# Kernel optimization log

Measured on AMD Instinct MI355X. Metric: run time of the kernel, lower is better.

The kernel has to match this reference:

```python
import jax, jax.numpy as jnp
import numpy as np

H = 2048   # hidden_size
NH = 16    # num_heads
D = 128    # head_dim_qk == head_dim_v
K = 4      # conv_kernel_size


def _causal_depthwise_conv(x, w, b):
    # x: [B,S,C], w: [C,K], b: [C]. Matches torch Conv1d(groups=C, padding=K-1)[..., :S]
    S = x.shape[1]
    xp = jnp.pad(x, ((0, 0), (K - 1, 0), (0, 0)))
    y = b
    for j in range(K):
        y = y + xp[:, j:j + S, :] * w[:, j]
    return y


def setup_inputs() -> dict:
    key = jax.random.key(0)
    ks = jax.random.split(key, 18)
    s = 0.02
    B, S = 2, 2048
    return {
        "x": jax.random.normal(ks[0], (B, S, H), dtype=jnp.float32),
        "Wq": jax.random.normal(ks[1], (H, NH * D), dtype=jnp.float32) * s,
        "Wk": jax.random.normal(ks[2], (H, NH * D), dtype=jnp.float32) * s,
        "Wv": jax.random.normal(ks[3], (H, NH * D), dtype=jnp.float32) * s,
        "Wa": jax.random.normal(ks[4], (H, NH), dtype=jnp.float32) * s,
        "ba": jax.random.normal(ks[5], (NH,), dtype=jnp.float32) * s,
        "Wb": jax.random.normal(ks[6], (H, NH), dtype=jnp.float32) * s,
        "bb": jax.random.normal(ks[7], (NH,), dtype=jnp.float32) * s,
        "Wg": jax.random.normal(ks[8], (H, NH * D), dtype=jnp.float32) * s,
        "Wo": jax.random.normal(ks[9], (NH * D, H), dtype=jnp.float32) * s,
        "qcw": jax.random.normal(ks[10], (NH * D, K), dtype=jnp.float32) * s,
        "qcb": jax.random.normal(ks[11], (NH * D,), dtype=jnp.float32) * s,
        "kcw": jax.random.normal(ks[12], (NH * D, K), dtype=jnp.float32) * s,
        "kcb": jax.random.normal(ks[13], (NH * D,), dtype=jnp.float32) * s,
        "vcw": jax.random.normal(ks[14], (NH * D, K), dtype=jnp.float32) * s,
        "vcb": jax.random.normal(ks[15], (NH * D,), dtype=jnp.float32) * s,
        "ln_w": jnp.ones((D,), dtype=jnp.float32),
        "ln_b": jnp.zeros((D,), dtype=jnp.float32),
    }


def _forward(x, Wq, Wk, Wv, Wa, ba, Wb, bb, Wg, Wo,
             qcw, qcb, kcw, kcb, vcw, vcb, ln_w, ln_b):
    B, S, _ = x.shape
    q = _causal_depthwise_conv(x @ Wq, qcw, qcb)
    k = _causal_depthwise_conv(x @ Wk, kcw, kcb)
    v = _causal_depthwise_conv(x @ Wv, vcw, vcb)
    q = jax.nn.silu(q).reshape(B, S, NH, D)
    k = jax.nn.silu(k).reshape(B, S, NH, D) * (D ** -0.5)
    v = jax.nn.silu(v).reshape(B, S, NH, D)
    alpha = jax.nn.sigmoid(x @ Wa + ba)  # [B,S,NH]
    beta = jax.nn.sigmoid(x @ Wb + bb)   # [B,S,NH]

    # time-major for scan
    qt = jnp.moveaxis(q, 1, 0)       # [S,B,NH,D]
    kt = jnp.moveaxis(k, 1, 0)
    vt = jnp.moveaxis(v, 1, 0)
    at = jnp.moveaxis(alpha, 1, 0)   # [S,B,NH]
    bt = jnp.moveaxis(beta, 1, 0)

    def step(St, inp):
        q_, k_, v_, a_, b_ = inp
        sk = jnp.einsum('bhij,bhj->bhi', St, k_)            # [B,NH,D]
        err = sk - v_
        Sn = (a_[..., None, None] * St
              - b_[..., None, None] * err[..., None] * k_[..., None, :])
        o_ = jnp.einsum('bhij,bhj->bhi', Sn, q_)
        return Sn, o_

    S0 = jnp.zeros((B, NH, D, D), dtype=x.dtype)
    _, o = jax.lax.scan(step, S0, (qt, kt, vt, at, bt))
    o = jnp.moveaxis(o, 0, 1)  # [B,S,NH,D]

    # LayerNorm over head_dim
    mu = jnp.mean(o, axis=-1, keepdims=True)
    var = jnp.mean(jnp.square(o - mu), axis=-1, keepdims=True)
    o = (o - mu) * jax.lax.rsqrt(var + 1e-5) * ln_w + ln_b

    g = jax.nn.sigmoid(x @ Wg).reshape(B, S, NH, D)
    o = (o * g).reshape(B, S, NH * D)
    return o @ Wo


def reference(x, Wq, Wk, Wv, Wa, ba, Wb, bb, Wg, Wo,
              qcw, qcb, kcw, kcb, vcw, vcb, ln_w, ln_b):
    return _forward(x, Wq, Wk, Wv, Wa, ba, Wb, bb, Wg, Wo,
                    qcw, qcb, kcw, kcb, vcw, vcb, ln_w, ln_b)
```

## Files before the change

### kernel.cpp

```cpp
#include <hip/hip_runtime.h>
#include <math.h>
#include <stdint.h>

typedef unsigned short u16;
typedef unsigned int u32;
typedef __attribute__((ext_vector_type(8))) short short8;
typedef __attribute__((ext_vector_type(4))) float f32x4;

#define MFMA16(a, b, c) __builtin_amdgcn_mfma_f32_16x16x32_bf16(a, b, c, 0, 0, 0)

__device__ __forceinline__ u16 f2bf(float f) {
  union { float f; u32 u; } v; v.f = f;
  return (u16)((v.u + 0x7FFFu + ((v.u >> 16) & 1u)) >> 16);
}
__device__ __forceinline__ float bf2f(u16 h) {
  union { u32 u; float f; } v; v.u = ((u32)h) << 16; return v.f;
}
__device__ __forceinline__ float bflo(u32 p) {
  union { u32 u; float f; } v; v.u = p << 16; return v.f;
}
__device__ __forceinline__ float bfhi(u32 p) {
  union { u32 u; float f; } v; v.u = p & 0xffff0000u; return v.f;
}
__device__ __forceinline__ float sigm(float x) { return 1.f / (1.f + expf(-x)); }

__global__ void k_cvt_x(const float* __restrict__ x, u16* __restrict__ xb) {
  int i = (blockIdx.x * 256 + threadIdx.x) * 8;
  float4 a = *(const float4*)(x + i);
  float4 b = *(const float4*)(x + i + 4);
  uint4 p;
  p.x = (u32)f2bf(a.x) | ((u32)f2bf(a.y) << 16);
  p.y = (u32)f2bf(a.z) | ((u32)f2bf(a.w) << 16);
  p.z = (u32)f2bf(b.x) | ((u32)f2bf(b.y) << 16);
  p.w = (u32)f2bf(b.z) | ((u32)f2bf(b.w) << 16);
  *(uint4*)(xb + i) = p;
}

__global__ void k_tconv4(const float* __restrict__ W0, const float* __restrict__ W1,
                         const float* __restrict__ W2, const float* __restrict__ W3,
                         u16* __restrict__ Wt) {
  __shared__ float tile[32][33];
  int z = blockIdx.z;
  const float* W = (z == 0) ? W0 : (z == 1) ? W1 : (z == 2) ? W2 : W3;
  u16* dst = Wt + (size_t)z * 2048 * 2048;
  int n0 = blockIdx.x * 32, k0 = blockIdx.y * 32;
  int tc = threadIdx.x & 31, tr = threadIdx.x >> 5;
  #pragma unroll
  for (int p = 0; p < 4; ++p) {
    int k = k0 + p * 8 + tr;
    tile[p * 8 + tr][tc] = W[(size_t)k * 2048 + n0 + tc];
  }
  __syncthreads();
  #pragma unroll
  for (int p = 0; p < 4; ++p) {
    int n = n0 + p * 8 + tr;
    dst[(size_t)n * 2048 + k0 + tc] = f2bf(tile[tc][p * 8 + tr]);
  }
}

__global__ void k_tconv(const float* __restrict__ W, u16* __restrict__ Wt) {
  __shared__ float tile[32][33];
  int n0 = blockIdx.x * 32, k0 = blockIdx.y * 32;
  int tc = threadIdx.x & 31, tr = threadIdx.x >> 5;
  #pragma unroll
  for (int p = 0; p < 4; ++p) {
    int k = k0 + p * 8 + tr;
    tile[p * 8 + tr][tc] = W[(size_t)k * 2048 + n0 + tc];
  }
  __syncthreads();
  #pragma unroll
  for (int p = 0; p < 4; ++p) {
    int n = n0 + p * 8 + tr;
    Wt[(size_t)n * 2048 + k0 + tc] = f2bf(tile[tc][p * 8 + tr]);
  }
}

__global__ __launch_bounds__(256)
void k_ab(const float* __restrict__ x, const float* __restrict__ Wa,
          const float* __restrict__ ba, const float* __restrict__ Wb,
          const float* __restrict__ bb, float* __restrict__ ab2) {
  __shared__ float Wl[128 * 32];
  __shared__ float xl[8][128];
  const int t = threadIdx.x;
  const int lr = t >> 5, c = t & 31;
  const int r0 = blockIdx.x * 8;
  const int ch = c & 15;
  const float* Wsrc = (c < 16) ? Wa : Wb;
  float acc = 0.f;
  for (int kt = 0; kt < 16; ++kt) {
    #pragma unroll
    for (int i = 0; i < 16; ++i) {
      int idx = i * 256 + t;
      int kk = idx >> 5, cc = idx & 31;
      const float* Ws = (cc < 16) ? Wa : Wb;
      Wl[kk * 32 + cc] = Ws[(kt * 128 + kk) * 16 + (cc & 15)];
    }
    #pragma unroll
    for (int i = 0; i < 4; ++i) {
      int idx = i * 256 + t;
      int rr = idx >> 7, kk = idx & 127;
      xl[rr][kk] = x[(size_t)(r0 + rr) * 2048 + kt * 128 + kk];
    }
    __syncthreads();
    #pragma unroll
    for (int kk = 0; kk < 128; kk += 4) {
      float2 x01 = *(const float2*)&xl[lr][kk];
      float2 x23 = *(const float2*)&xl[lr][kk + 2];
      acc += x01.x * Wl[(kk + 0) * 32 + c] + x01.y * Wl[(kk + 1) * 32 + c]
           + x23.x * Wl[(kk + 2) * 32 + c] + x23.y * Wl[(kk + 3) * 32 + c];
    }
    __syncthreads();
  }
  acc += (c < 16) ? ba[ch] : bb[ch];
  float sg = sigm(acc);
  int rowi = r0 + lr;
  int b = rowi >> 11, s = rowi & 2047;
  size_t base = ((size_t)(b * 16 + ch) * 2048 + s) * 2;
  if (c < 16) ab2[base + 0] = sg;
  else        ab2[base + 1] = sg;
}

__device__ __forceinline__ void gld_lds16(const u16* g, u16* l) {
  __builtin_amdgcn_global_load_lds((const __attribute__((address_space(1))) void*)g,
                                   (__attribute__((address_space(3))) void*)l, 16, 0, 0);
}

template <int MODE>
__global__ void k_gemm(const u16* __restrict__ A, const u16* __restrict__ Bw,
                       void* C0, void* C1, int Kd) {
  __shared__ u16 As[2][128 * 32];
  __shared__ u16 Bs[2][128 * 32];
  const int t = threadIdx.x;
  const int lane = t & 63, wv = t >> 6;
  const int wr = wv >> 1, wc = wv & 1;
  const int m0 = blockIdx.y * 128, n0 = blockIdx.x * 128;
  f32x4 acc[4][4] = {};
  const int NT = Kd / 32;

  auto stage = [&](int buf, int kt) {
    #pragma unroll
    for (int i = 0; i < 2; ++i) {
      int li = i * 256 + t;
      int row = li >> 2, kc = li & 3;
      int kcs = kc ^ ((row >> 1) & 3);
      const u16* ga = A + (size_t)(m0 + row) * Kd + kt * 32 + kcs * 8;
      gld_lds16(ga, &As[buf][(i * 256 + wv * 64) * 8]);
      const u16* gb = Bw + (size_t)(n0 + row) * Kd + kt * 32 + kcs * 8;
      gld_lds16(gb, &Bs[buf][(i * 256 + wv * 64) * 8]);
    }
  };

  stage(0, 0);
  __syncthreads();
  int buf = 0;
  const int l15 = lane & 15, l4 = lane >> 4;
  for (int kt = 0; kt < NT; ++kt) {
    if (kt + 1 < NT) stage(buf ^ 1, kt + 1);
    short8 af[4], bfr[4];
    #pragma unroll
    for (int m = 0; m < 4; ++m) {
      int row = wr * 64 + m * 16 + l15;
      int g = l4 ^ ((row >> 1) & 3);
      af[m] = *(const short8*)&As[buf][row * 32 + g * 8];
    }
    #pragma unroll
    for (int n = 0; n < 4; ++n) {
      int row = wc * 64 + n * 16 + l15;
      int g = l4 ^ ((row >> 1) & 3);
      bfr[n] = *(const short8*)&Bs[buf][row * 32 + g * 8];
    }
    #pragma unroll
    for (int m = 0; m < 4; ++m)
      #pragma unroll
      for (int n = 0; n < 4; ++n)
        acc[m][n] = MFMA16(af[m], bfr[n], acc[m][n]);
    __syncthreads();
    buf ^= 1;
  }
  #pragma unroll
  for (int m = 0; m < 4; ++m)
    #pragma unroll
    for (int n = 0; n < 4; ++n)
      #pragma unroll
      for (int e = 0; e < 4; ++e) {
        int row = m0 + wr * 64 + m * 16 + l4 * 4 + e;
        int col = n0 + wc * 64 + n * 16 + l15;
        if (MODE == 0) {
          ((float*)C0)[(size_t)row * 2048 + col] = acc[m][n][e];
        } else {
          u16 vb = f2bf(acc[m][n][e]);
          if (n0 < 6144) ((u16*)C0)[(size_t)row * 6144 + col] = vb;
          else           ((u16*)C1)[(size_t)row * 2048 + (col - 6144)] = vb;
        }
      }
}

template <int MODE>
__global__ __launch_bounds__(512)
void k_gemm8(const u16* __restrict__ A, const u16* __restrict__ Bw,
             void* C0, void* C1) {
  __shared__ u16 lds[65536];
  const int t = threadIdx.x;
  const int w = t >> 6, lane = t & 63;
  const int l15 = lane & 15, l4 = lane >> 4;
  const int wm = w >> 2, wn = w & 3;
  const int bid = blockIdx.x;
  const int mt = ((bid & 7) << 1) | ((bid >> 3) & 1);
  const int nt = bid >> 4;
  const int m0 = mt * 256, n0 = nt * 256;

  f32x4 acc[8][4] = {};
  short8 a[4][2], b[4][2];

  auto stageHalf = [&](int buf, int kt, int mat, int half) {
    const u16* src = mat ? Bw : A;
    const int row0 = (mat ? n0 : m0) + half * 128;
    u16* dst0 = &lds[mat * 32768 + (buf * 2 + half) * 8192 + w * 1024];
    #pragma unroll
    for (int i = 0; i < 2; ++i) {
      int f = w * 128 + i * 64 + lane;
      int rr = f >> 3, g = f & 7;
      const u16* ga = src + (size_t)(row0 + rr) * 2048 + kt * 64 + ((g ^ (rr & 7)) << 3);
      gld_lds16(ga, dst0 + i * 512);
    }
  };
  auto rdA = [&](int buf, int mq, int ks) {
    int row = wm * 64 + (mq & 3) * 16 + l15;
    int g = (l4 + ks * 4) ^ (row & 7);
    return *(const short8*)&lds[(buf * 2 + (mq >> 2)) * 8192 + row * 64 + g * 8];
  };
  auto rdB = [&](int buf, int n, int ks) {
    int row = wn * 32 + (n & 1) * 16 + l15;
    int g = (l4 + ks * 4) ^ (row & 7);
    return *(const short8*)&lds[32768 + (buf * 2 + (n >> 1)) * 8192 + row * 64 + g * 8];
  };

  stageHalf(0, 0, 0, 0); stageHalf(0, 0, 1, 0);
  stageHalf(0, 0, 1, 1); stageHalf(0, 0, 0, 1);
  asm volatile("s_waitcnt vmcnt(0)" ::: "memory");
  __builtin_amdgcn_s_barrier();
  __builtin_amdgcn_sched_barrier(0);

  for (int kt = 0; kt < 32; ++kt) {
    const int bufc = kt & 1, bufn = bufc ^ 1;
    const int ktn = (kt + 1 < 32) ? kt + 1 : 31;

    #pragma unroll
    for (int mq = 0; mq < 4; ++mq) { a[mq][0] = rdA(bufc, mq, 0); a[mq][1] = rdA(bufc, mq, 1); }
    #pragma unroll
    for (int n = 0; n < 2; ++n) { b[n][0] = rdB(bufc, n, 0); b[n][1] = rdB(bufc, n, 1); }
    stageHalf(bufn, ktn, 0, 0);
    __builtin_amdgcn_s_barrier();
    asm volatile("s_waitcnt lgkmcnt(0)" ::: "memory");
    __builtin_amdgcn_sched_barrier(0);
    __builtin_amdgcn_s_setprio(1);
    #pragma unroll
    for (int mq = 0; mq < 4; ++mq)
      #pragma unroll
      for (int n = 0; n < 2; ++n) {
        acc[mq][n] = MFMA16(a[mq][0], b[n][0], acc[mq][n]);
        acc[mq][n] = MFMA16(a[mq][1], b[n][1], acc[mq][n]);
      }
    __builtin_amdgcn_s_setprio(0);
    asm volatile("s_waitcnt vmcnt(4)" ::: "memory");
    __builtin_amdgcn_s_barrier();
    __builtin_amdgcn_sched_barrier(0);

    #pragma unroll
    for (int n = 2; n < 4; ++n) { b[n][0] = rdB(bufc, n, 0); b[n][1] = rdB(bufc, n, 1); }
    stageHalf(bufn, ktn, 1, 0);
    __builtin_amdgcn_s_barrier();
    asm volatile("s_waitcnt lgkmcnt(0)" ::: "memory");
    __builtin_amdgcn_sched_barrier(0);
    __builtin_amdgcn_s_setprio(1);
    #pragma unroll
    for (int mq = 0; mq < 4; ++mq)
      #pragma unroll
      for (int n = 2; n < 4; ++n) {
        acc[mq][n] = MFMA16(a[mq][0], b[n][0], acc[mq][n]);
        acc[mq][n] = MFMA16(a[mq][1], b[n][1], acc[mq][n]);
      }
    __builtin_amdgcn_s_setprio(0);
    asm volatile("s_waitcnt vmcnt(4)" ::: "memory");
    __builtin_amdgcn_s_barrier();
    __builtin_amdgcn_sched_barrier(0);

    #pragma unroll
    for (int mq = 0; mq < 4; ++mq) { a[mq][0] = rdA(bufc, mq + 4, 0); a[mq][1] = rdA(bufc, mq + 4, 1); }
    stageHalf(bufn, ktn, 1, 1);
    __builtin_amdgcn_s_barrier();
    asm volatile("s_waitcnt lgkmcnt(0)" ::: "memory");
    __builtin_amdgcn_sched_barrier(0);
    __builtin_amdgcn_s_setprio(1);
    #pragma unroll
    for (int mq = 0; mq < 4; ++mq)
      #pragma unroll
      for (int n = 2; n < 4; ++n) {
        acc[mq + 4][n] = MFMA16(a[mq][0], b[n][0], acc[mq + 4][n]);
        acc[mq + 4][n] = MFMA16(a[mq][1], b[n][1], acc[mq + 4][n]);
      }
    __builtin_amdgcn_s_setprio(0);
    __builtin_amdgcn_s_barrier();
    __builtin_amdgcn_sched_barrier(0);

    stageHalf(bufn, ktn, 0, 1);
    __builtin_amdgcn_s_barrier();
    asm volatile("s_waitcnt lgkmcnt(0)" ::: "memory");
    __builtin_amdgcn_sched_barrier(0);
    __builtin_amdgcn_s_setprio(1);
    #pragma unroll
    for (int mq = 0; mq < 4; ++mq)
      #pragma unroll
      for (int n = 0; n < 2; ++n) {
        acc[mq + 4][n] = MFMA16(a[mq][0], b[n][0], acc[mq + 4][n]);
        acc[mq + 4][n] = MFMA16(a[mq][1], b[n][1], acc[mq + 4][n]);
      }
    __builtin_amdgcn_s_setprio(0);
    asm volatile("s_waitcnt vmcnt(4)" ::: "memory");
    __builtin_amdgcn_s_barrier();
    __builtin_amdgcn_sched_barrier(0);
  }

  const bool toG = (MODE == 1) && (n0 >= 6144);
  #pragma unroll
  for (int mq = 0; mq < 8; ++mq) {
    int row = m0 + (mq >> 2) * 128 + wm * 64 + (mq & 3) * 16 + l4 * 4;
    #pragma unroll
    for (int n = 0; n < 4; ++n) {
      int col = n0 + (n >> 1) * 128 + wn * 32 + (n & 1) * 16 + l15;
      #pragma unroll
      for (int e = 0; e < 4; ++e) {
        if (MODE == 0) {
          ((float*)C0)[(size_t)(row + e) * 2048 + col] = acc[mq][n][e];
        } else {
          u16 vb = f2bf(acc[mq][n][e]);
          if (!toG) ((u16*)C0)[(size_t)(row + e) * 6144 + col] = vb;
          else      ((u16*)C1)[(size_t)(row + e) * 2048 + (col - 6144)] = vb;
        }
      }
    }
  }
}

__global__ void k_conv(const u16* __restrict__ projQKV,
                       const float* __restrict__ qcw, const float* __restrict__ qcb,
                       const float* __restrict__ kcw, const float* __restrict__ kcb,
                       const float* __restrict__ vcw, const float* __restrict__ vcb,
                       u16* __restrict__ qkv2) {
  int idx = blockIdx.x * 256 + threadIdx.x;
  int cq = idx % 1536, rrow = idx / 1536;
  int c = cq * 4;
  int s = rrow & 2047, b = rrow >> 11;
  int type = c >> 11;
  int ch = c & 2047;
  int h = ch >> 7, d = ch & 127;
  const float* cw; const float* cb;
  if (type == 0)      { cw = qcw; cb = qcb; }
  else if (type == 1) { cw = kcw; cb = kcb; }
  else                { cw = vcw; cb = vcb; }
  float wch[4][4];
  #pragma unroll
  for (int u = 0; u < 4; ++u) {
    float4 wv = *(const float4*)(cw + (ch + u) * 4);
    wch[u][0] = wv.x; wch[u][1] = wv.y; wch[u][2] = wv.z; wch[u][3] = wv.w;
  }
  float4 bv = *(const float4*)(cb + ch);
  float accv[4] = {bv.x, bv.y, bv.z, bv.w};
  #pragma unroll
  for (int j = 0; j < 4; ++j) {
    int sj = s - 3 + j;
    if (sj < 0) continue;
    const u16* p = projQKV + (size_t)(rrow + j - 3) * 6144 + c;
    u32 pa = *(const u32*)p;
    u32 pb = *(const u32*)(p + 2);
    accv[0] += bflo(pa) * wch[0][j];
    accv[1] += bfhi(pa) * wch[1][j];
    accv[2] += bflo(pb) * wch[2][j];
    accv[3] += bfhi(pb) * wch[3][j];
  }
  u16 o4[4];
  #pragma unroll
  for (int u = 0; u < 4; ++u) {
    float y = accv[u];
    float sv = y * sigm(y);
    if (type == 1) sv *= 0.08838834764831845f;
    o4[u] = f2bf(sv);
  }
  int off = (type == 1 ? 0 : (type == 0 ? 128 : 256)) + d;
  u16* dst = qkv2 + ((size_t)(b * 16 + h) * 2048 + s) * 384 + off;
  *(u32*)dst       = (u32)o4[0] | ((u32)o4[1] << 16);
  *(u32*)(dst + 2) = (u32)o4[2] | ((u32)o4[3] << 16);
}

__global__ __launch_bounds__(256)
void k_chunkA(const u16* __restrict__ qkv2, const float* __restrict__ ab2,
              u16* __restrict__ Tbv, u16* __restrict__ nTbk,
              u16* __restrict__ Aq, float* __restrict__ vecs,
              u16* __restrict__ Kt) {
  __shared__ u16 Kl[64][136], Ql[64][136];
  __shared__ float Gk[4096], Gq[4096];
  __shared__ float clL[64], laL[64], bL[64], gpL[64];
  const int unit = blockIdx.x;
  const int bh = unit >> 5, c = unit & 31;
  const int t = threadIdx.x;
  const int wv = t >> 6, lane = t & 63;
  const int l15 = lane & 15, l4 = lane >> 4;
  const u16* qb = qkv2 + ((size_t)bh * 2048 + c * 64) * 384;

  #pragma unroll
  for (int p = 0; p < 4; ++p) {
    int ld = p * 256 + t;
    int row = ld >> 4, c8 = (ld & 15) * 8;
    *(uint4*)&Kl[row][c8] = *(const uint4*)(qb + (size_t)row * 384 + c8);
    *(uint4*)&Ql[row][c8] = *(const uint4*)(qb + (size_t)row * 384 + 128 + c8);
  }
  if (wv == 0) {
    float2 abv = *(const float2*)(ab2 + ((size_t)bh * 2048 + c * 64 + lane) * 2);
    float la = log2f(abv.x);
    float cl = la;
    #pragma unroll
    for (int o = 1; o < 64; o <<= 1) {
      float nv = __shfl_up(cl, o, 64);
      if (lane >= o) cl += nv;
    }
    clL[lane] = cl; laL[lane] = la; bL[lane] = abv.y;
    gpL[lane] = exp2f(cl - la);
  }
  __syncthreads();

  {
    const int t0 = (wv >> 1) * 32, i0 = (wv & 1) * 32;
    f32x4 ak[2][2] = {}, aq[2][2] = {};
    #pragma unroll
    for (int ks = 0; ks < 4; ++ks) {
      short8 bk[2], Ka[2], Qa[2];
      #pragma unroll
      for (int n = 0; n < 2; ++n)
        bk[n] = *(const short8*)&Kl[i0 + n * 16 + l15][ks * 32 + l4 * 8];
      #pragma unroll
      for (int m = 0; m < 2; ++m) {
        Ka[m] = *(const short8*)&Kl[t0 + m * 16 + l15][ks * 32 + l4 * 8];
        Qa[m] = *(const short8*)&Ql[t0 + m * 16 + l15][ks * 32 + l4 * 8];
      }
      #pragma unroll
      for (int m = 0; m < 2; ++m)
        #pragma unroll
        for (int n = 0; n < 2; ++n) {
          ak[m][n] = MFMA16(Ka[m], bk[n], ak[m][n]);
          aq[m][n] = MFMA16(Qa[m], bk[n], aq[m][n]);
        }
    }
    #pragma unroll
    for (int m = 0; m < 2; ++m)
      #pragma unroll
      for (int n = 0; n < 2; ++n)
        #pragma unroll
        for (int e = 0; e < 4; ++e) {
          int row = t0 + m * 16 + l4 * 4 + e;
          int col = i0 + n * 16 + l15;
          Gk[row * 64 + col] = ak[m][n][e];
          Gq[row * 64 + col] = aq[m][n][e];
        }
  }
  __syncthreads();

  #pragma unroll
  for (int p = 0; p < 16; ++p) {
    int e = p * 256 + t; int tt = e >> 6, ii = e & 63;
    float lv = 0.f;
    if (ii < tt) lv = bL[tt] * Gk[e] * exp2f(clL[tt] - laL[tt] - clL[ii]);
    float av = (ii <= tt) ? Gq[e] * exp2f(clL[tt] - clL[ii]) : 0.f;
    Gk[e] = lv;
    Aq[(size_t)unit * 4096 + e] = f2bf(av);
  }
  __syncthreads();

  float X[64];
  if (t < 128) {
    #pragma unroll
    for (int r = 0; r < 64; ++r)
      X[r] = bL[r] * bf2f(qb[(size_t)r * 384 + 256 + t]);
  } else {
    int ck = t - 128;
    #pragma unroll
    for (int r = 0; r < 64; ++r)
      X[r] = -bL[r] * gpL[r] * bf2f(Kl[r][ck]);
  }
  #pragma unroll
  for (int i = 0; i < 63; ++i) {
    float xi = X[i];
    #pragma unroll
    for (int r = i + 1; r < 64; ++r)
      X[r] = fmaf(-Gk[r * 64 + i], xi, X[r]);
  }
  if (t < 128) {
    #pragma unroll
    for (int r = 0; r < 64; ++r)
      Tbv[(size_t)unit * 8192 + r * 128 + t] = f2bf(X[r]);
  } else {
    #pragma unroll
    for (int r = 0; r < 64; ++r)
      nTbk[(size_t)unit * 8192 + r * 128 + (t - 128)] = f2bf(X[r]);
  }
  if (t < 64) {
    vecs[(size_t)unit * 128 + t] = exp2f(clL[t]);
    vecs[(size_t)unit * 128 + 64 + t] = exp2f(clL[63] - clL[t]);
  }
  {
    int dk = t >> 1, tt0 = (t & 1) * 32;
    uint4 w[4];
    u16* wp = (u16*)w;
    #pragma unroll
    for (int j = 0; j < 32; ++j) wp[j] = Kl[tt0 + j][dk];
    uint4* dst = (uint4*)(Kt + (size_t)unit * 8192 + dk * 64 + tt0);
    dst[0] = w[0]; dst[1] = w[1]; dst[2] = w[2]; dst[3] = w[3];
  }
}

#define OFF_NT  0
#define OFF_AQ  8192
#define OFF_Q   12288
#define OFF_KT  20480
#define OFF_TBV 28672
#define STG_U16 29696

__global__ __launch_bounds__(256)
void k_chunkB(const u16* __restrict__ qkv2, const u16* __restrict__ Tbv,
              const u16* __restrict__ nTbk, const u16* __restrict__ Aq,
              const u16* __restrict__ Kt, const float* __restrict__ vecs,
              float* __restrict__ o) {
  __shared__ u16 stg[2][STG_U16];
  __shared__ float S[16 * 132];
  __shared__ u16 Ut[16 * 72], Utd[16 * 72];
  __shared__ float gdl[2][128];
  const int bid = blockIdx.x;
  const int xcd = bid & 7, within = bid >> 3;
  const int sl = within & 7, hgrp = within >> 3;
  const int bh = hgrp * 8 + xcd;
  const int dv0 = sl * 16;
  const int b = bh >> 4, h = bh & 15;
  const int t = threadIdx.x;
  const int wv = t >> 6, lane = t & 63;
  const int l15 = lane & 15, l4 = lane >> 4;
  const int t0 = wv * 16;
  const int dk0 = wv * 32;
  const u16* qbase = qkv2 + (size_t)bh * 2048 * 384;
  float* obase = o + (size_t)b * 2048 * 2048 + h * 128 + dv0;

  for (int p = t; p < 16 * 132; p += 256) S[p] = 0.f;

  auto stage = [&](int buf, int c) {
    u16* sb = &stg[buf][0];
    const size_t unit = (size_t)bh * 32 + c;
    const u16* tbk = nTbk + unit * 8192;
    const u16* aqp = Aq + unit * 4096;
    const u16* ktp = Kt + unit * 8192;
    const u16* tbv = Tbv + unit * 8192;
    const u16* qp  = qbase + (size_t)c * 64 * 384 + 128;
    #pragma unroll
    for (int r = 0; r < 4; ++r) {
      int f = r * 256 + t; int rr = f >> 4, c16 = f & 15;
      gld_lds16(tbk + rr * 128 + (c16 ^ (rr & 7)) * 8, sb + OFF_NT + (r * 256 + wv * 64) * 8);
    }
    #pragma unroll
    for (int r = 0; r < 2; ++r) {
      int f = r * 256 + t; int rr = f >> 3, c8 = f & 7;
      gld_lds16(aqp + rr * 64 + (c8 ^ (rr & 7)) * 8, sb + OFF_AQ + (r * 256 + wv * 64) * 8);
    }
    #pragma unroll
    for (int r = 0; r < 4; ++r) {
      int f = r * 256 + t; int rr = f >> 4, c16 = f & 15;
      gld_lds16(qp + rr * 384 + (c16 ^ (rr & 7)) * 8, sb + OFF_Q + (r * 256 + wv * 64) * 8);
    }
    #pragma unroll
    for (int r = 0; r < 4; ++r) {
      int f = r * 256 + t; int rr = f >> 3, c8 = f & 7;
      gld_lds16(ktp + rr * 64 + (c8 ^ (rr & 7)) * 8, sb + OFF_KT + (r * 256 + wv * 64) * 8);
    }
    if (t < 128)
      gld_lds16(tbv + (t >> 1) * 128 + dv0 + (t & 1) * 8, sb + OFF_TBV + wv * 64 * 8);
  };

  stage(0, 0);
  if (t < 128) gdl[0][t] = vecs[(size_t)bh * 32 * 128 + t];
  __syncthreads();

  for (int c = 0; c < 32; ++c) {
    const int buf = c & 1;
    const u16* sb = &stg[buf][0];
    float vnext = 0.f;
    if (c + 1 < 32) {
      stage(buf ^ 1, c + 1);
      if (t < 128) vnext = vecs[((size_t)bh * 32 + c + 1) * 128 + t];
    }

    f32x4 acc1 = {}, acc2 = {};
    #pragma unroll
    for (int e = 0; e < 4; ++e)
      acc1[e] = bf2f(sb[OFF_TBV + (t0 + l4 * 4 + e) * 16 + l15]);
    #pragma unroll
    for (int ks = 0; ks < 4; ++ks) {
      short8 bhi, blo;
      {
        const float* srow = &S[l15 * 132 + ks * 32 + l4 * 8];
        float4 s0 = *(const float4*)srow, s1 = *(const float4*)(srow + 4);
        float sv[8] = {s0.x, s0.y, s0.z, s0.w, s1.x, s1.y, s1.z, s1.w};
        #pragma unroll
        for (int j = 0; j < 8; ++j) {
          u16 hv = f2bf(sv[j]);
          bhi[j] = (short)hv;
          blo[j] = (short)f2bf(sv[j] - bf2f(hv));
        }
      }
      const int cx = ((ks * 4 + l4) ^ (l15 & 7)) * 8;
      short8 a1 = *(const short8*)&sb[OFF_NT + (t0 + l15) * 128 + cx];
      short8 a2 = *(const short8*)&sb[OFF_Q + (t0 + l15) * 128 + cx];
      acc1 = MFMA16(a1, bhi, acc1);
      acc1 = MFMA16(a1, blo, acc1);
      acc2 = MFMA16(a2, bhi, acc2);
      acc2 = MFMA16(a2, blo, acc2);
    }
    {
      u16 up[4], ud[4];
      #pragma unroll
      for (int e = 0; e < 4; ++e) {
        float uv = acc1[e];
        up[e] = f2bf(uv);
        ud[e] = f2bf(uv * gdl[buf][64 + t0 + l4 * 4 + e]);
      }
      int ux = l15 * 72 + t0 + l4 * 4;
      *(u32*)&Ut[ux]      = (u32)up[0] | ((u32)up[1] << 16);
      *(u32*)&Ut[ux + 2]  = (u32)up[2] | ((u32)up[3] << 16);
      *(u32*)&Utd[ux]     = (u32)ud[0] | ((u32)ud[1] << 16);
      *(u32*)&Utd[ux + 2] = (u32)ud[2] | ((u32)ud[3] << 16);
    }
    asm volatile("s_waitcnt lgkmcnt(0)" ::: "memory");
    __builtin_amdgcn_s_barrier();
    __builtin_amdgcn_sched_barrier(0);

    #pragma unroll
    for (int e = 0; e < 4; ++e) acc2[e] *= gdl[buf][t0 + l4 * 4 + e];
    #pragma unroll
    for (int ks = 0; ks < 2; ++ks) {
      const int cx = ((ks * 4 + l4) ^ (l15 & 7)) * 8;
      short8 af = *(const short8*)&sb[OFF_AQ + (t0 + l15) * 64 + cx];
      short8 bf_ = *(const short8*)&Ut[l15 * 72 + ks * 32 + l4 * 8];
      acc2 = MFMA16(af, bf_, acc2);
    }
    #pragma unroll
    for (int e = 0; e < 4; ++e)
      obase[(size_t)(c * 64 + t0 + l4 * 4 + e) * 2048 + l15] = acc2[e];

    f32x4 acc3[2] = {};
    #pragma unroll
    for (int ks = 0; ks < 2; ++ks) {
      short8 a3 = *(const short8*)&Utd[l15 * 72 + ks * 32 + l4 * 8];
      #pragma unroll
      for (int n = 0; n < 2; ++n) {
        const int kr = dk0 + n * 16 + l15;
        const int cx = ((ks * 4 + l4) ^ (l15 & 7)) * 8;
        short8 b3 = *(const short8*)&sb[OFF_KT + kr * 64 + cx];
        acc3[n] = MFMA16(a3, b3, acc3[n]);
      }
    }
    float gtot = gdl[buf][63];
    #pragma unroll
    for (int n = 0; n < 2; ++n)
      #pragma unroll
      for (int e = 0; e < 4; ++e) {
        float* sp = &S[(l4 * 4 + e) * 132 + dk0 + n * 16 + l15];
        *sp = gtot * *sp + acc3[n][e];
      }
    if (c + 1 < 32 && t < 128) gdl[buf ^ 1][t] = vnext;
    __syncthreads();
  }
}

__global__ void k_lng(const float* __restrict__ o, const u16* __restrict__ projG,
                      const float* __restrict__ ln_w, const float* __restrict__ ln_b,
                      u16* __restrict__ og) {
  int gidx = blockIdx.x * 4 + (threadIdx.x >> 6);
  int lane = threadIdx.x & 63;
  int rrow = gidx >> 4, h = gidx & 15;
  const float* op = o + (size_t)rrow * 2048 + h * 128;
  float2 x2 = *(const float2*)(op + lane * 2);
  float sum = x2.x + x2.y, sq = x2.x * x2.x + x2.y * x2.y;
  #pragma unroll
  for (int m = 1; m < 64; m <<= 1) {
    sum += __shfl_xor(sum, m, 64);
    sq  += __shfl_xor(sq, m, 64);
  }
  float mu = sum * (1.f / 128.f);
  float var = sq * (1.f / 128.f) - mu * mu;
  float rs = 1.0f / sqrtf(var + 1e-5f);
  u32 gu = *(const u32*)(projG + (size_t)rrow * 2048 + h * 128 + lane * 2);
  float g0 = sigm(bflo(gu)), g1 = sigm(bfhi(gu));
  int d0 = lane * 2;
  float y0 = ((x2.x - mu) * rs * ln_w[d0] + ln_b[d0]) * g0;
  float y1 = ((x2.y - mu) * rs * ln_w[d0 + 1] + ln_b[d0 + 1]) * g1;
  *(u32*)(og + (size_t)rrow * 2048 + h * 128 + d0) = (u32)f2bf(y0) | ((u32)f2bf(y1) << 16);
}

extern "C" void kernel_launch(void* const* d_in, const int* in_sizes, int n_in,
                              void* d_out, int out_size, void* d_ws, size_t ws_size,
                              hipStream_t stream) {
  const float* x   = (const float*)d_in[0];
  const float* Wq  = (const float*)d_in[1];
  const float* Wk  = (const float*)d_in[2];
  const float* Wv  = (const float*)d_in[3];
  const float* Wa  = (const float*)d_in[4];
  const float* ba  = (const float*)d_in[5];
  const float* Wb  = (const float*)d_in[6];
  const float* bb  = (const float*)d_in[7];
  const float* Wg  = (const float*)d_in[8];
  const float* Wo  = (const float*)d_in[9];
  const float* qcw = (const float*)d_in[10];
  const float* qcb = (const float*)d_in[11];
  const float* kcw = (const float*)d_in[12];
  const float* kcb = (const float*)d_in[13];
  const float* vcw = (const float*)d_in[14];
  const float* vcb = (const float*)d_in[15];
  const float* lnw = (const float*)d_in[16];
  const float* lnb = (const float*)d_in[17];
  float* out = (float*)d_out;

  if (ws_size < 168820736ull) return;
  char* ws = (char*)d_ws;
  u16*   xb   = (u16*)(ws);
  u16*   Kt   = (u16*)(ws);
  u16*   og   = (u16*)(ws);
  u16*   Wt   = (u16*)(ws + 16777216);
  u16*   Wot  = (u16*)(ws + 16777216);
  u16*   Tbv  = (u16*)(ws + 25165824);
  u16*   Aq   = (u16*)(ws + 41943040);
  u16*   pQKV = (u16*)(ws + 50331648);
  float* oB   = (float*)(ws + 50331648);
  u16*   nTbk = (u16*)(ws + 83886080);
  u16*   pG   = (u16*)(ws + 100663296);
  u16*   qkv2 = (u16*)(ws + 117440512);
  float* ab2  = (float*)(ws + 167772160);
  float* vecs = (float*)(ws + 168296448);

  k_cvt_x<<<4096, 256, 0, stream>>>(x, xb);
  k_tconv4<<<dim3(64, 64, 4), 256, 0, stream>>>(Wq, Wk, Wv, Wg, Wt);
  k_ab<<<512, 256, 0, stream>>>(x, Wa, ba, Wb, bb, ab2);

  k_gemm8<1><<<512, 512, 0, stream>>>(xb, Wt, pQKV, pG);
  k_tconv<<<dim3(64, 64), 256, 0, stream>>>(Wo, Wot);
  k_conv<<<24576, 256, 0, stream>>>(pQKV, qcw, qcb, kcw, kcb, vcw, vcb, qkv2);
  k_chunkA<<<1024, 256, 0, stream>>>(qkv2, ab2, Tbv, nTbk, Aq, vecs, Kt);
  k_chunkB<<<256, 256, 0, stream>>>(qkv2, Tbv, nTbk, Aq, Kt, vecs, oB);
  k_lng<<<16384, 256, 0, stream>>>(oB, pG, lnw, lnb, og);
  k_gemm<0><<<dim3(16, 32), 256, 0, stream>>>(og, Wot, out, nullptr, 2048);
}
```

Before: 466.9 us.

## Restructure GEMM main loop into two phases with fewer barriers

Restructures the GEMM k-loop from four sub-phases with eight barriers per iteration to two phases. Three of the four next-tile stage loads now issue up front and the last goes out mid-iteration, each followed by a larger MFMA block covering all four B fragments. The aim is to cut barrier and lgkmcnt wait overhead and give the scheduler bigger MFMA runs. In exchange the code holds all B fragments in registers at once and relies on the vmcnt(6)/vmcnt(2) counts being right. Removing the explicit lgkmcnt waits and intermediate barriers risks LDS read/write ordering hazards between buffers. It also drops an unused variable in k_ab.

```diff
diff --git a/kernel.cpp b/kernel.cpp
--- a/kernel.cpp
+++ b/kernel.cpp
@@ -85,7 +85,6 @@
   const int lr = t >> 5, c = t & 31;
   const int r0 = blockIdx.x * 8;
   const int ch = c & 15;
-  const float* Wsrc = (c < 16) ? Wa : Wb;
   float acc = 0.f;
   for (int kt = 0; kt < 16; ++kt) {
     #pragma unroll
@@ -245,78 +244,39 @@
     const int bufc = kt & 1, bufn = bufc ^ 1;
     const int ktn = (kt + 1 < 32) ? kt + 1 : 31;
 
+    stageHalf(bufn, ktn, 0, 0);
+    stageHalf(bufn, ktn, 1, 0);
+    stageHalf(bufn, ktn, 1, 1);
     #pragma unroll
     for (int mq = 0; mq < 4; ++mq) { a[mq][0] = rdA(bufc, mq, 0); a[mq][1] = rdA(bufc, mq, 1); }
     #pragma unroll
-    for (int n = 0; n < 2; ++n) { b[n][0] = rdB(bufc, n, 0); b[n][1] = rdB(bufc, n, 1); }
-    stageHalf(bufn, ktn, 0, 0);
-    __builtin_amdgcn_s_barrier();
-    asm volatile("s_waitcnt lgkmcnt(0)" ::: "memory");
-    __builtin_amdgcn_sched_barrier(0);
+    for (int n = 0; n < 4; ++n) { b[n][0] = rdB(bufc, n, 0); b[n][1] = rdB(bufc, n, 1); }
     __builtin_amdgcn_s_setprio(1);
     #pragma unroll
     for (int mq = 0; mq < 4; ++mq)
       #pragma unroll
-      for (int n = 0; n < 2; ++n) {
+      for (int n = 0; n < 4; ++n) {
         acc[mq][n] = MFMA16(a[mq][0], b[n][0], acc[mq][n]);
         acc[mq][n] = MFMA16(a[mq][1], b[n][1], acc[mq][n]);
       }
     __builtin_amdgcn_s_setprio(0);
-    asm volatile("s_waitcnt vmcnt(4)" ::: "memory");
+    asm volatile("s_waitcnt vmcnt(6)" ::: "memory");
     __builtin_amdgcn_s_barrier();
     __builtin_amdgcn_sched_barrier(0);
 
-    #pragma unroll
-    for (int n = 2; n < 4; ++n) { b[n][0] = rdB(bufc, n, 0); b[n][1] = rdB(bufc, n, 1); }
-    stageHalf(bufn, ktn, 1, 0);
-    __builtin_amdgcn_s_barrier();
-    asm volatile("s_waitcnt lgkmcnt(0)" ::: "memory");
-    __builtin_amdgcn_sched_barrier(0);
+    stageHalf(bufn, ktn, 0, 1);
+    #pragma unroll
+    for (int mq = 0; mq < 4; ++mq) { a[mq][0] = rdA(bufc, mq + 4, 0); a[mq][1] = rdA(bufc, mq + 4, 1); }
     __builtin_amdgcn_s_setprio(1);
     #pragma unroll
     for (int mq = 0; mq < 4; ++mq)
       #pragma unroll
-      for (int n = 2; n < 4; ++n) {
-        acc[mq][n] = MFMA16(a[mq][0], b[n][0], acc[mq][n]);
-        acc[mq][n] = MFMA16(a[mq][1], b[n][1], acc[mq][n]);
-      }
-    __builtin_amdgcn_s_setprio(0);
-    asm volatile("s_waitcnt vmcnt(4)" ::: "memory");
-    __builtin_amdgcn_s_barrier();
-    __builtin_amdgcn_sched_barrier(0);
-
-    #pragma unroll
-    for (int mq = 0; mq < 4; ++mq) { a[mq][0] = rdA(bufc, mq + 4, 0); a[mq][1] = rdA(bufc, mq + 4, 1); }
-    stageHalf(bufn, ktn, 1, 1);
-    __builtin_amdgcn_s_barrier();
-    asm volatile("s_waitcnt lgkmcnt(0)" ::: "memory");
-    __builtin_amdgcn_sched_barrier(0);
-    __builtin_amdgcn_s_setprio(1);
-    #pragma unroll
-    for (int mq = 0; mq < 4; ++mq)
-      #pragma unroll
-      for (int n = 2; n < 4; ++n) {
+      for (int n = 0; n < 4; ++n) {
         acc[mq + 4][n] = MFMA16(a[mq][0], b[n][0], acc[mq + 4][n]);
         acc[mq + 4][n] = MFMA16(a[mq][1], b[n][1], acc[mq + 4][n]);
       }
     __builtin_amdgcn_s_setprio(0);
-    __builtin_amdgcn_s_barrier();
-    __builtin_amdgcn_sched_barrier(0);
-
-    stageHalf(bufn, ktn, 0, 1);
-    __builtin_amdgcn_s_barrier();
-    asm volatile("s_waitcnt lgkmcnt(0)" ::: "memory");
-    __builtin_amdgcn_sched_barrier(0);
-    __builtin_amdgcn_s_setprio(1);
-    #pragma unroll
-    for (int mq = 0; mq < 4; ++mq)
-      #pragma unroll
-      for (int n = 0; n < 2; ++n) {
-        acc[mq + 4][n] = MFMA16(a[mq][0], b[n][0], acc[mq + 4][n]);
-        acc[mq + 4][n] = MFMA16(a[mq][1], b[n][1], acc[mq + 4][n]);
-      }
-    __builtin_amdgcn_s_setprio(0);
-    asm volatile("s_waitcnt vmcnt(4)" ::: "memory");
+    asm volatile("s_waitcnt vmcnt(2)" ::: "memory");
     __builtin_amdgcn_s_barrier();
     __builtin_amdgcn_sched_barrier(0);
   }
```

Result: no change. 465.5 us (-0.3%).
